# Kernel tuning notes

Measured on AMD Instinct MI355X. Metric: run time of the kernel, lower is better.

## Reference

```python
import jax, jax.numpy as jnp
import numpy as np

ALPHA = 1.0
BETA = 0.25
NUM_EMBEDS = 8192
EMBED_DIM = 512
B, T = 32, 256


def setup_inputs() -> dict:
    key = jax.random.key(0)
    k1, k2 = jax.random.split(key)
    z_e = jax.random.normal(k1, (B, EMBED_DIM, T), dtype=jnp.float32)
    codebook = jax.random.normal(k2, (NUM_EMBEDS, EMBED_DIM), dtype=jnp.float32)
    return {"z_e": z_e, "codebook": codebook}


def reference(z_e, codebook):
    # z_e: (b, d, t) -> (b, t, d)
    z = jnp.transpose(z_e, (0, 2, 1))
    b, t, d = z.shape
    flat = z.reshape(-1, d)  # (N, d), N = b*t

    # squared euclidean distances to every codebook vector: (N, K)
    dists = (
        jnp.sum(flat * flat, axis=1, keepdims=True)
        + jnp.sum(codebook * codebook, axis=1)
        - 2.0 * flat @ codebook.T
    )
    idx = jnp.argmin(dists, axis=1)  # (N,)

    # codebook lookup (equivalent to one-hot @ codebook)
    z_q = codebook[idx].reshape(b, t, d)

    # commitment loss (codebook is EMA-updated, so only e_latent term)
    e_latent_loss = jnp.mean((jax.lax.stop_gradient(z_q) - z) ** 2)
    vq_loss = ALPHA * BETA * e_latent_loss

    # straight-through estimator
    z_q_st = z + jax.lax.stop_gradient(z_q - z)
    z_q_out = jnp.transpose(z_q_st, (0, 2, 1))  # back to (b, d, t)

    # perplexity from mean one-hot assignment probabilities
    counts = jnp.zeros((codebook.shape[0],), dtype=jnp.float32).at[idx].add(1.0)
    avg_probs = counts / flat.shape[0]
    perplexity = jnp.exp(-jnp.sum(avg_probs * jnp.log(avg_probs + 1e-10)))

    return z_q_out, vq_loss, perplexity
```

## Files before the change

kernel.cpp:

```cpp
#include <hip/hip_runtime.h>
#include <stdint.h>

typedef _Float16 half8 __attribute__((ext_vector_type(8)));
typedef float floatx16 __attribute__((ext_vector_type(16)));
typedef unsigned long long u64;

#define ALPHA_ 1.0f
#define BETA_ 0.25f
#define NUM_EMBEDS 8192
#define EMBED_DIM 512
#define B_ 32
#define T_ 256
#define N_TOK 8192
#define THR_GAP 2e-3f


typedef __attribute__((address_space(1))) const void ga_void;
typedef __attribute__((address_space(3))) void ls_void;
__device__ __forceinline__ void gl_lds16(const void* g, void* l) {
    __builtin_amdgcn_global_load_lds((ga_void*)g, (ls_void*)l, 16, 0, 0);
}

__device__ __forceinline__ uint32_t mono(float s) {
    uint32_t u = __float_as_uint(s);
    return (u & 0x80000000u) ? ~u : (u | 0x80000000u);
}
__device__ __forceinline__ float unmono(uint32_t v) {
    return __uint_as_float((v & 0x80000000u) ? (v ^ 0x80000000u) : ~v);
}

__global__ void pack_cb_kernel(const float* __restrict__ cb, _Float16* __restrict__ ci,
                               float* __restrict__ cnorm) {
    int row = blockIdx.x * 4 + (threadIdx.x >> 6);
    int lane = threadIdx.x & 63;
    const float* src = cb + (size_t)row * EMBED_DIM + lane * 8;
    float4 v0 = *(const float4*)src;
    float4 v1 = *(const float4*)(src + 4);
    float x[8] = {v0.x, v0.y, v0.z, v0.w, v1.x, v1.y, v1.z, v1.w};
    half8 hh, mm;
    float s = 0.f;
#pragma unroll
    for (int j = 0; j < 8; ++j) {
        s += x[j] * x[j];
        _Float16 hv = (_Float16)x[j];
        hh[j] = hv;
        mm[j] = (_Float16)((x[j] - (float)hv) * 2048.0f);
    }
    _Float16* dst = ci + (size_t)row * 1024 + lane * 16;
    *(half8*)dst = hh;
    *(half8*)(dst + 8) = mm;
#pragma unroll
    for (int d = 32; d; d >>= 1) s += __shfl_xor(s, d, 64);
    if (lane == 0) cnorm[row] = s;
}

__global__ void pack_z_kernel(const float* __restrict__ z, _Float16* __restrict__ zi) {
    int tid = threadIdx.x;
    int lane = tid & 63, ds = tid >> 6;
    int b = blockIdx.x >> 2;
    int t = ((blockIdx.x & 3) << 6) + lane;
    size_t n = (size_t)b * T_ + t;
    for (int g = 0; g < 16; ++g) {
        int d0 = g * 32 + ds * 8;
        const float* src = z + ((size_t)b * EMBED_DIM + d0) * T_ + t;
        half8 hh, mm;
#pragma unroll
        for (int j = 0; j < 8; ++j) {
            float x = -2.0f * src[(size_t)j * T_];
            _Float16 hv = (_Float16)x;
            hh[j] = hv;
            mm[j] = (_Float16)((x - (float)hv) * 2048.0f);
        }
        _Float16* dst = zi + n * 1024 + (size_t)(g * 4 + ds) * 16;
        *(half8*)dst = hh;
        *(half8*)(dst + 8) = mm;
    }
}

#define MFMA16(a, b, c) __builtin_amdgcn_mfma_f32_32x32x16_f16(a, b, c, 0, 0, 0)

__global__ __launch_bounds__(256, 2) void argmin_kernel(
    const _Float16* __restrict__ cb_i, const _Float16* __restrict__ zt_i,
    const float* __restrict__ cnorm, u64* __restrict__ slot_m1,
    _Float16* __restrict__ slot_d) {
    __shared__ _Float16 As[2][8192];
    __shared__ _Float16 Bs[2][8192];
    __shared__ u64 sK[128];
    __shared__ float sV1[128], sV2[128];
    const int tid = threadIdx.x;
    const int l = tid & 63;
    const int wv = tid >> 6;
    const int l31 = l & 31;
    const int hf = l >> 5;
    const int wp = wv >> 1, wq = wv & 1;
    const int n0 = blockIdx.x * 128;
    const int c0 = blockIdx.y * 128;

    const bool isA = wv < 2;
    const _Float16* gsrc = isA ? cb_i : zt_i;
    const int rbase = (isA ? c0 : n0) + ((wv & 1) << 6);
    const int srow = l >> 3;
    const int sseg = (l & 7) ^ srow;
    const size_t lanefix = (size_t)(rbase + srow) * 1024 + sseg * 8;

    floatx16 acc1[2][2], acc2[2][2];
#pragma unroll
    for (int a = 0; a < 2; ++a)
#pragma unroll
        for (int b = 0; b < 2; ++b)
#pragma unroll
            for (int r = 0; r < 16; ++r) { acc1[a][b][r] = 0.f; acc2[a][b][r] = 0.f; }

    auto stage = [&](int p, int s) {
        const _Float16* gs = gsrc + lanefix + (size_t)s * 64;
        _Float16* lb = (isA ? As[p] : Bs[p]) + ((wv & 1) << 12);
#pragma unroll
        for (int j = 0; j < 8; ++j)
            gl_lds16(gs + (size_t)j * 8192, lb + j * 512);
    };

    stage(0, 0);
    __syncthreads();
    for (int s = 0; s < 16; ++s) {
        const int p = s & 1;
        if (s < 15) stage(p ^ 1, s + 1);
        const _Float16* Ab = As[p] + (wp * 64 + l31) * 64;
        const _Float16* Bb = Bs[p] + (wq * 64 + l31) * 64;
        const int rs = l31 & 7;
#pragma unroll
        for (int kk = 0; kk < 2; ++kk) {
            const int j = kk * 2 + hf;
            const int ph = ((2 * j) ^ rs) * 8;
            const int pm = ((2 * j + 1) ^ rs) * 8;
            half8 Ah0 = *(const half8*)(Ab + ph), Am0 = *(const half8*)(Ab + pm);
            half8 Ah1 = *(const half8*)(Ab + 2048 + ph), Am1 = *(const half8*)(Ab + 2048 + pm);
            half8 Bh0 = *(const half8*)(Bb + ph), Bm0 = *(const half8*)(Bb + pm);
            half8 Bh1 = *(const half8*)(Bb + 2048 + ph), Bm1 = *(const half8*)(Bb + 2048 + pm);
            acc1[0][0] = MFMA16(Ah0, Bh0, acc1[0][0]);
            acc2[0][0] = MFMA16(Ah0, Bm0, acc2[0][0]);
            acc2[0][0] = MFMA16(Am0, Bh0, acc2[0][0]);
            acc1[0][1] = MFMA16(Ah0, Bh1, acc1[0][1]);
            acc2[0][1] = MFMA16(Ah0, Bm1, acc2[0][1]);
            acc2[0][1] = MFMA16(Am0, Bh1, acc2[0][1]);
            acc1[1][0] = MFMA16(Ah1, Bh0, acc1[1][0]);
            acc2[1][0] = MFMA16(Ah1, Bm0, acc2[1][0]);
            acc2[1][0] = MFMA16(Am1, Bh0, acc2[1][0]);
            acc1[1][1] = MFMA16(Ah1, Bh1, acc1[1][1]);
            acc2[1][1] = MFMA16(Ah1, Bm1, acc2[1][1]);
            acc2[1][1] = MFMA16(Am1, Bh1, acc2[1][1]);
        }
        __syncthreads();
    }

    u64 km[2]; float kv1[2], kv2[2];
#pragma unroll
    for (int qi = 0; qi < 2; ++qi) {
        u64 m1k = ~0ULL;
        float m1v = 3.4e38f, m2 = 3.4e38f;
#pragma unroll
        for (int ti = 0; ti < 2; ++ti)
#pragma unroll
            for (int g = 0; g < 4; ++g) {
                const int cb4 = c0 + wp * 64 + ti * 32 + g * 8 + hf * 4;
                float4 cn = *(const float4*)(cnorm + cb4);
                const floatx16& A1 = acc1[ti][qi];
                const floatx16& A2 = acc2[ti][qi];
                float sv[4] = {cn.x + A1[g * 4 + 0] + A2[g * 4 + 0] * (1.0f / 2048.0f),
                               cn.y + A1[g * 4 + 1] + A2[g * 4 + 1] * (1.0f / 2048.0f),
                               cn.z + A1[g * 4 + 2] + A2[g * 4 + 2] * (1.0f / 2048.0f),
                               cn.w + A1[g * 4 + 3] + A2[g * 4 + 3] * (1.0f / 2048.0f)};
#pragma unroll
                for (int q = 0; q < 4; ++q) {
                    u64 key = ((u64)mono(sv[q]) << 32) | (uint32_t)(cb4 + q);
                    if (key < m1k) { m2 = m1v; m1v = sv[q]; m1k = key; }
                    else m2 = fminf(m2, sv[q]);
                }
            }
        u64 ok = __shfl_xor(m1k, 32, 64);
        float ov = __shfl_xor(m1v, 32, 64);
        float om2 = __shfl_xor(m2, 32, 64);
        if (ok < m1k) { m2 = fminf(fminf(m2, om2), m1v); m1v = ov; m1k = ok; }
        else m2 = fminf(fminf(m2, om2), ov);
        km[qi] = m1k; kv1[qi] = m1v; kv2[qi] = m2;
    }
    if (wp == 1 && hf == 0) {
#pragma unroll
        for (int qi = 0; qi < 2; ++qi) {
            int idx = wq * 64 + qi * 32 + l31;
            sK[idx] = km[qi]; sV1[idx] = kv1[qi]; sV2[idx] = kv2[qi];
        }
    }
    __syncthreads();
    if (wp == 0 && hf == 0) {
#pragma unroll
        for (int qi = 0; qi < 2; ++qi) {
            int idx = wq * 64 + qi * 32 + l31;
            u64 m1k = km[qi]; float m1v = kv1[qi], m2 = kv2[qi];
            u64 ok = sK[idx]; float ov = sV1[idx], om2 = sV2[idx];
            if (ok < m1k) { m2 = fminf(fminf(m2, om2), m1v); m1v = ov; m1k = ok; }
            else m2 = fminf(fminf(m2, om2), ov);
            int tok = n0 + idx;
            slot_m1[((size_t)blockIdx.y << 13) + tok] = m1k;
            slot_d[((size_t)blockIdx.y << 13) + tok] = (_Float16)(m2 - m1v);
        }
    }
}

__global__ void combine_kernel(const u64* __restrict__ slot_m1, const _Float16* __restrict__ slot_d,
                               u64* __restrict__ wexact, int* __restrict__ worklist,
                               int* __restrict__ nflag) {
    int tok = blockIdx.x * 256 + threadIdx.x;
    u64 g1 = ~0ULL;
    float g1v = 3.4e38f, g2 = 3.4e38f;
    for (int c = 0; c < 64; ++c) {
        u64 k = slot_m1[((size_t)c << 13) + tok];
        float kv = unmono((uint32_t)(k >> 32));
        float v2 = kv + (float)slot_d[((size_t)c << 13) + tok];
        if (k < g1) { g2 = fminf(g2, g1v); g1 = k; g1v = kv; }
        else g2 = fminf(g2, kv);
        g2 = fminf(g2, v2);
    }
    if (g2 - g1v > THR_GAP) wexact[tok] = g1;
    else { int i = atomicAdd(nflag, 1); if (i < 8192) worklist[i] = tok; }
}

__global__ void fallback_kernel(const float* __restrict__ z, const float* __restrict__ cb,
                                const float* __restrict__ cnorm,
                                const int* __restrict__ worklist, const int* __restrict__ nflag,
                                u64* __restrict__ wexact) {
    int n = *nflag;
    if (n > 8192) n = 8192;
    const int l = threadIdx.x & 63, wv = threadIdx.x >> 6;
    const int cbase = blockIdx.x * 128;
    for (int fi = blockIdx.y; fi < n; fi += gridDim.y) {
        int tok = worklist[fi];
        int b = tok >> 8, t = tok & 255;
        const float* zp = z + ((size_t)b * EMBED_DIM) * T_ + t;
        float zr[8];
#pragma unroll
        for (int j = 0; j < 8; ++j) zr[j] = zp[(size_t)(l * 8 + j) * T_];
        u64 m1 = ~0ULL;
        for (int j = 0; j < 32; ++j) {
            int c = cbase + wv + j * 4;
            const float* cp = cb + (size_t)c * EMBED_DIM + l * 8;
            float4 a = *(const float4*)cp, bb = *(const float4*)(cp + 4);
            float dot = zr[0] * a.x + zr[1] * a.y + zr[2] * a.z + zr[3] * a.w +
                        zr[4] * bb.x + zr[5] * bb.y + zr[6] * bb.z + zr[7] * bb.w;
#pragma unroll
            for (int m = 32; m; m >>= 1) dot += __shfl_xor(dot, m, 64);
            if (l == 0) {
                float s = cnorm[c] - 2.0f * dot;
                u64 key = ((u64)mono(s) << 32) | (uint32_t)c;
                if (key < m1) m1 = key;
            }
        }
        if (l == 0) atomicMin(&wexact[tok], m1);
    }
}

__global__ void gather_kernel(const float* __restrict__ z, const float* __restrict__ cb,
                              const u64* __restrict__ wexact,
                              float* __restrict__ out, int* __restrict__ counts,
                              float* __restrict__ sse_acc) {
    __shared__ unsigned int sIdx[64];
    __shared__ float red[4];
    const int tid = threadIdx.x;
    const int n0 = blockIdx.x * 64;
    const int b = n0 >> 8;
    const int t0 = n0 & 255;
    if (tid < 64) {
        unsigned int idx = (unsigned int)(wexact[n0 + tid] & 0xffffffffULL);
        sIdx[tid] = idx;
        atomicAdd(&counts[idx], 1);
    }
    __syncthreads();
    const int w = tid >> 6;
    const int lane = tid & 63;
    const float* crow = cb + (size_t)sIdx[lane] * EMBED_DIM;
    const size_t base = ((size_t)b * EMBED_DIM) * T_ + (size_t)(t0 + lane);
    float sse = 0.f;
    for (int d = w; d < EMBED_DIM; d += 4) {
        float v = crow[d];
        size_t o = base + (size_t)d * T_;
        float diff = v - z[o];
        out[o] = v;
        sse += diff * diff;
    }
    for (int m = 32; m; m >>= 1) sse += __shfl_xor(sse, m, 64);
    if (lane == 0) red[w] = sse;
    __syncthreads();
    if (tid == 0) atomicAdd(sse_acc, red[0] + red[1] + red[2] + red[3]);
}

__global__ void finalize_kernel(const int* __restrict__ counts,
                                const float* __restrict__ sse_acc,
                                float* __restrict__ out) {
    __shared__ float red[4];
    const int tid = threadIdx.x;
    float e = 0.f;
    for (int k = tid; k < NUM_EMBEDS; k += 256) {
        float p = (float)counts[k] * (1.0f / (float)N_TOK);
        e += p * logf(p + 1e-10f);
    }
    for (int m = 32; m; m >>= 1) e += __shfl_xor(e, m, 64);
    if ((tid & 63) == 0) red[tid >> 6] = e;
    __syncthreads();
    if (tid == 0) {
        float ent = red[0] + red[1] + red[2] + red[3];
        size_t off = (size_t)B_ * EMBED_DIM * T_;
        out[off + 0] = (ALPHA_ * BETA_) * sse_acc[0] / (float)((size_t)N_TOK * EMBED_DIM);
        out[off + 1] = expf(-ent);
    }
}

extern "C" void kernel_launch(void* const* d_in, const int* in_sizes, int n_in,
                              void* d_out, int out_size, void* d_ws, size_t ws_size,
                              hipStream_t stream) {
    const float* z = (const float*)d_in[0];
    const float* cb = (const float*)d_in[1];
    float* out = (float*)d_out;
    char* ws = (char*)d_ws;
    u64* wexact = (u64*)ws;
    float* cnorm = (float*)(ws + 65536);
    int* counts = (int*)(ws + 98304);
    float* sse = (float*)(ws + 131072);
    int* nflag = (int*)(ws + 131076);
    int* worklist = (int*)(ws + 131080);
    u64* slot_m1 = (u64*)(ws + (1ull << 20));
    _Float16* slot_d = (_Float16*)(ws + (5ull << 20));
    _Float16* cb_i = (_Float16*)(ws + (6ull << 20));
    _Float16* zt_i = (_Float16*)(ws + (22ull << 20));

    hipMemsetAsync(wexact, 0xFF, NUM_EMBEDS * sizeof(u64), stream);
    hipMemsetAsync(counts, 0, NUM_EMBEDS * sizeof(int) + 8, stream);

    pack_cb_kernel<<<NUM_EMBEDS / 4, 256, 0, stream>>>(cb, cb_i, cnorm);
    pack_z_kernel<<<N_TOK / 64, 256, 0, stream>>>(z, zt_i);
    argmin_kernel<<<dim3(N_TOK / 128, NUM_EMBEDS / 128), 256, 0, stream>>>(cb_i, zt_i, cnorm, slot_m1, slot_d);
    combine_kernel<<<N_TOK / 256, 256, 0, stream>>>(slot_m1, slot_d, wexact, worklist, nflag);
    fallback_kernel<<<dim3(64, 16), 256, 0, stream>>>(z, cb, cnorm, worklist, nflag, wexact);
    gather_kernel<<<N_TOK / 64, 256, 0, stream>>>(z, cb, wexact, out, counts, sse);
    finalize_kernel<<<1, 256, 0, stream>>>(counts, sse, out);
}
```

Measured before the change: 363.5 us.

## Enlarge argmin tile to 256x128 with 8 waves and ping-pong MFMA scheduling

The argmin GEMM block tile grows from 128x128 to 256 codebook rows by 128 tokens, using 512 threads (8 waves) and a single fused 96KB double-buffered LDS region loaded by all waves. The k-loop is split into two half-steps, with explicit s_barrier, waitcnt and setprio so waves alternate between LDS reads and MFMA bursts while the global-to-LDS prefetch is in flight. The cross-wave reduction now merges four wave rows, and combine_kernel reads 32 partial slots instead of 64. This aims for more operand reuse per loaded byte and better overlap of loads with matrix math, at the cost of heavier LDS use, lower occupancy and fragile hand-placed barriers.

```diff
diff --git a/kernel.cpp b/kernel.cpp
--- a/kernel.cpp
+++ b/kernel.cpp
@@ -79,29 +79,35 @@
 
 #define MFMA16(a, b, c) __builtin_amdgcn_mfma_f32_32x32x16_f16(a, b, c, 0, 0, 0)
 
-__global__ __launch_bounds__(256, 2) void argmin_kernel(
+__global__ __launch_bounds__(512, 2) void argmin_kernel(
     const _Float16* __restrict__ cb_i, const _Float16* __restrict__ zt_i,
     const float* __restrict__ cnorm, u64* __restrict__ slot_m1,
     _Float16* __restrict__ slot_d) {
-    __shared__ _Float16 As[2][8192];
-    __shared__ _Float16 Bs[2][8192];
-    __shared__ u64 sK[128];
-    __shared__ float sV1[128], sV2[128];
+    __shared__ alignas(16) _Float16 Sm[2][24576];
+    __shared__ u64 sK[3][128];
+    __shared__ float sV1[3][128], sV2[3][128];
+
     const int tid = threadIdx.x;
     const int l = tid & 63;
     const int wv = tid >> 6;
     const int l31 = l & 31;
     const int hf = l >> 5;
-    const int wp = wv >> 1, wq = wv & 1;
+    const int wm = wv >> 1;
+    const int wn = wv & 1;
     const int n0 = blockIdx.x * 128;
-    const int c0 = blockIdx.y * 128;
-
-    const bool isA = wv < 2;
-    const _Float16* gsrc = isA ? cb_i : zt_i;
-    const int rbase = (isA ? c0 : n0) + ((wv & 1) << 6);
+    const int c0 = blockIdx.y * 256;
+
     const int srow = l >> 3;
     const int sseg = (l & 7) ^ srow;
-    const size_t lanefix = (size_t)(rbase + srow) * 1024 + sseg * 8;
+    const _Float16* gsrc[6];
+#pragma unroll
+    for (int j = 0; j < 6; ++j) {
+        int c = wv * 6 + j;
+        gsrc[j] = (c < 32)
+                      ? cb_i + (size_t)(c0 + c * 8 + srow) * 1024 + sseg * 8
+                      : zt_i + (size_t)(n0 + (c - 32) * 8 + srow) * 1024 + sseg * 8;
+    }
+    const int sloff = wv * 3072;
 
     floatx16 acc1[2][2], acc2[2][2];
 #pragma unroll
@@ -111,31 +117,42 @@
 #pragma unroll
             for (int r = 0; r < 16; ++r) { acc1[a][b][r] = 0.f; acc2[a][b][r] = 0.f; }
 
-    auto stage = [&](int p, int s) {
-        const _Float16* gs = gsrc + lanefix + (size_t)s * 64;
-        _Float16* lb = (isA ? As[p] : Bs[p]) + ((wv & 1) << 12);
-#pragma unroll
-        for (int j = 0; j < 8; ++j)
-            gl_lds16(gs + (size_t)j * 8192, lb + j * 512);
-    };
-
-    stage(0, 0);
-    __syncthreads();
-    for (int s = 0; s < 16; ++s) {
-        const int p = s & 1;
-        if (s < 15) stage(p ^ 1, s + 1);
-        const _Float16* Ab = As[p] + (wp * 64 + l31) * 64;
-        const _Float16* Bb = Bs[p] + (wq * 64 + l31) * 64;
-        const int rs = l31 & 7;
-#pragma unroll
-        for (int kk = 0; kk < 2; ++kk) {
-            const int j = kk * 2 + hf;
-            const int ph = ((2 * j) ^ rs) * 8;
-            const int pm = ((2 * j + 1) ^ rs) * 8;
-            half8 Ah0 = *(const half8*)(Ab + ph), Am0 = *(const half8*)(Ab + pm);
-            half8 Ah1 = *(const half8*)(Ab + 2048 + ph), Am1 = *(const half8*)(Ab + 2048 + pm);
-            half8 Bh0 = *(const half8*)(Bb + ph), Bm0 = *(const half8*)(Bb + pm);
-            half8 Bh1 = *(const half8*)(Bb + 2048 + ph), Bm1 = *(const half8*)(Bb + 2048 + pm);
+    const int rs = l31 & 7;
+    const int goh0 = ((2 * hf) ^ rs) * 8;
+    const int gom0 = ((2 * hf + 1) ^ rs) * 8;
+    const int goh1 = ((4 + 2 * hf) ^ rs) * 8;
+    const int gom1 = ((4 + 2 * hf + 1) ^ rs) * 8;
+    const int aoff = (wm * 64 + l31) * 64;
+    const int boff = 16384 + (wn * 64 + l31) * 64;
+
+#pragma unroll
+    for (int j = 0; j < 6; ++j) gl_lds16(gsrc[j], &Sm[0][sloff + j * 512]);
+    asm volatile("s_waitcnt vmcnt(0)" ::: "memory");
+    __builtin_amdgcn_s_barrier();
+
+    for (int t = 0; t < 16; ++t) {
+        const int p = t & 1;
+        const _Float16* Ap = &Sm[0][0] + p * 24576 + aoff;
+        const _Float16* Bp = &Sm[0][0] + p * 24576 + boff;
+        _Float16* snx = &Sm[0][0] + (p ^ 1) * 24576 + sloff;
+        {
+            half8 Ah0 = *(const half8*)(Ap + goh0);
+            half8 Am0 = *(const half8*)(Ap + gom0);
+            half8 Ah1 = *(const half8*)(Ap + 2048 + goh0);
+            half8 Am1 = *(const half8*)(Ap + 2048 + gom0);
+            half8 Bh0 = *(const half8*)(Bp + goh0);
+            half8 Bm0 = *(const half8*)(Bp + gom0);
+            half8 Bh1 = *(const half8*)(Bp + 2048 + goh0);
+            half8 Bm1 = *(const half8*)(Bp + 2048 + gom0);
+            if (t < 15) {
+#pragma unroll
+                for (int j = 0; j < 6; ++j)
+                    gl_lds16(gsrc[j] + (size_t)(t + 1) * 64, snx + j * 512);
+            }
+            __builtin_amdgcn_s_barrier();
+            asm volatile("s_waitcnt lgkmcnt(0)" ::: "memory");
+            __builtin_amdgcn_sched_barrier(0);
+            __builtin_amdgcn_s_setprio(1);
             acc1[0][0] = MFMA16(Ah0, Bh0, acc1[0][0]);
             acc2[0][0] = MFMA16(Ah0, Bm0, acc2[0][0]);
             acc2[0][0] = MFMA16(Am0, Bh0, acc2[0][0]);
@@ -148,8 +165,38 @@
             acc1[1][1] = MFMA16(Ah1, Bh1, acc1[1][1]);
             acc2[1][1] = MFMA16(Ah1, Bm1, acc2[1][1]);
             acc2[1][1] = MFMA16(Am1, Bh1, acc2[1][1]);
-        }
-        __syncthreads();
+            __builtin_amdgcn_s_setprio(0);
+            __builtin_amdgcn_s_barrier();
+        }
+        {
+            half8 Ah0 = *(const half8*)(Ap + goh1);
+            half8 Am0 = *(const half8*)(Ap + gom1);
+            half8 Ah1 = *(const half8*)(Ap + 2048 + goh1);
+            half8 Am1 = *(const half8*)(Ap + 2048 + gom1);
+            half8 Bh0 = *(const half8*)(Bp + goh1);
+            half8 Bm0 = *(const half8*)(Bp + gom1);
+            half8 Bh1 = *(const half8*)(Bp + 2048 + goh1);
+            half8 Bm1 = *(const half8*)(Bp + 2048 + gom1);
+            __builtin_amdgcn_s_barrier();
+            asm volatile("s_waitcnt lgkmcnt(0)" ::: "memory");
+            __builtin_amdgcn_sched_barrier(0);
+            __builtin_amdgcn_s_setprio(1);
+            acc1[0][0] = MFMA16(Ah0, Bh0, acc1[0][0]);
+            acc2[0][0] = MFMA16(Ah0, Bm0, acc2[0][0]);
+            acc2[0][0] = MFMA16(Am0, Bh0, acc2[0][0]);
+            acc1[0][1] = MFMA16(Ah0, Bh1, acc1[0][1]);
+            acc2[0][1] = MFMA16(Ah0, Bm1, acc2[0][1]);
+            acc2[0][1] = MFMA16(Am0, Bh1, acc2[0][1]);
+            acc1[1][0] = MFMA16(Ah1, Bh0, acc1[1][0]);
+            acc2[1][0] = MFMA16(Ah1, Bm0, acc2[1][0]);
+            acc2[1][0] = MFMA16(Am1, Bh0, acc2[1][0]);
+            acc1[1][1] = MFMA16(Ah1, Bh1, acc1[1][1]);
+            acc2[1][1] = MFMA16(Ah1, Bm1, acc2[1][1]);
+            acc2[1][1] = MFMA16(Am1, Bh1, acc2[1][1]);
+            __builtin_amdgcn_s_setprio(0);
+            asm volatile("s_waitcnt vmcnt(0)" ::: "memory");
+            __builtin_amdgcn_s_barrier();
+        }
     }
 
     u64 km[2]; float kv1[2], kv2[2];
@@ -161,7 +208,7 @@
         for (int ti = 0; ti < 2; ++ti)
 #pragma unroll
             for (int g = 0; g < 4; ++g) {
-                const int cb4 = c0 + wp * 64 + ti * 32 + g * 8 + hf * 4;
+                const int cb4 = c0 + wm * 64 + ti * 32 + g * 8 + hf * 4;
                 float4 cn = *(const float4*)(cnorm + cb4);
                 const floatx16& A1 = acc1[ti][qi];
                 const floatx16& A2 = acc2[ti][qi];
@@ -183,22 +230,25 @@
         else m2 = fminf(fminf(m2, om2), ov);
         km[qi] = m1k; kv1[qi] = m1v; kv2[qi] = m2;
     }
-    if (wp == 1 && hf == 0) {
+    if (wm != 0 && hf == 0) {
 #pragma unroll
         for (int qi = 0; qi < 2; ++qi) {
-            int idx = wq * 64 + qi * 32 + l31;
-            sK[idx] = km[qi]; sV1[idx] = kv1[qi]; sV2[idx] = kv2[qi];
+            int idx = wn * 64 + qi * 32 + l31;
+            sK[wm - 1][idx] = km[qi]; sV1[wm - 1][idx] = kv1[qi]; sV2[wm - 1][idx] = kv2[qi];
         }
     }
     __syncthreads();
-    if (wp == 0 && hf == 0) {
+    if (wm == 0 && hf == 0) {
 #pragma unroll
         for (int qi = 0; qi < 2; ++qi) {
-            int idx = wq * 64 + qi * 32 + l31;
+            int idx = wn * 64 + qi * 32 + l31;
             u64 m1k = km[qi]; float m1v = kv1[qi], m2 = kv2[qi];
-            u64 ok = sK[idx]; float ov = sV1[idx], om2 = sV2[idx];
-            if (ok < m1k) { m2 = fminf(fminf(m2, om2), m1v); m1v = ov; m1k = ok; }
-            else m2 = fminf(fminf(m2, om2), ov);
+#pragma unroll
+            for (int j = 0; j < 3; ++j) {
+                u64 ok = sK[j][idx]; float ov = sV1[j][idx], om2 = sV2[j][idx];
+                if (ok < m1k) { m2 = fminf(fminf(m2, om2), m1v); m1v = ov; m1k = ok; }
+                else m2 = fminf(fminf(m2, om2), ov);
+            }
             int tok = n0 + idx;
             slot_m1[((size_t)blockIdx.y << 13) + tok] = m1k;
             slot_d[((size_t)blockIdx.y << 13) + tok] = (_Float16)(m2 - m1v);
@@ -212,7 +262,7 @@
     int tok = blockIdx.x * 256 + threadIdx.x;
     u64 g1 = ~0ULL;
     float g1v = 3.4e38f, g2 = 3.4e38f;
-    for (int c = 0; c < 64; ++c) {
+    for (int c = 0; c < 32; ++c) {
         u64 k = slot_m1[((size_t)c << 13) + tok];
         float kv = unmono((uint32_t)(k >> 32));
         float v2 = kv + (float)slot_d[((size_t)c << 13) + tok];
@@ -336,7 +386,7 @@
 
     pack_cb_kernel<<<NUM_EMBEDS / 4, 256, 0, stream>>>(cb, cb_i, cnorm);
     pack_z_kernel<<<N_TOK / 64, 256, 0, stream>>>(z, zt_i);
-    argmin_kernel<<<dim3(N_TOK / 128, NUM_EMBEDS / 128), 256, 0, stream>>>(cb_i, zt_i, cnorm, slot_m1, slot_d);
+    argmin_kernel<<<dim3(N_TOK / 128, NUM_EMBEDS / 256), 512, 0, stream>>>(cb_i, zt_i, cnorm, slot_m1, slot_d);
     combine_kernel<<<N_TOK / 256, 256, 0, stream>>>(slot_m1, slot_d, wexact, worklist, nflag);
     fallback_kernel<<<dim3(64, 16), 256, 0, stream>>>(z, cb, cnorm, worklist, nflag, wexact);
     gather_kernel<<<N_TOK / 64, 256, 0, stream>>>(z, cb, wexact, out, counts, sse);
```

Result: slower. 376.5 us (+3.6%).

## Load MFMA fragments directly from pre-swizzled global layout instead of LDS staging

Applied to the files above, without the earlier changes.

Packing kernels now write codebook and token data in an MFMA-fragment-ordered layout, so each lane reads its half8 operands directly from global memory with contiguous per-lane addresses. The argmin kernel drops LDS double buffering and its barriers, and uses 512-thread blocks where each of 8 waves owns 32 codebook rows against 128 tokens, with register double-buffered loads. Per-block codebook coverage doubles to 256, which halves the number of partial slots the combine kernel reduces. This trades LDS traffic and syncs for repeated global/L2 reads of the token tile across waves and exposed global latency.

```diff
diff --git a/kernel.cpp b/kernel.cpp
--- a/kernel.cpp
+++ b/kernel.cpp
@@ -15,12 +15,6 @@
 #define THR_GAP 2e-3f
 
 
-typedef __attribute__((address_space(1))) const void ga_void;
-typedef __attribute__((address_space(3))) void ls_void;
-__device__ __forceinline__ void gl_lds16(const void* g, void* l) {
-    __builtin_amdgcn_global_load_lds((ga_void*)g, (ls_void*)l, 16, 0, 0);
-}
-
 __device__ __forceinline__ uint32_t mono(float s) {
     uint32_t u = __float_as_uint(s);
     return (u & 0x80000000u) ? ~u : (u | 0x80000000u);
@@ -29,11 +23,11 @@
     return __uint_as_float((v & 0x80000000u) ? (v ^ 0x80000000u) : ~v);
 }
 
-__global__ void pack_cb_kernel(const float* __restrict__ cb, _Float16* __restrict__ ci,
+__global__ void pack_cb_kernel(const float* __restrict__ cb, _Float16* __restrict__ cf,
                                float* __restrict__ cnorm) {
     int row = blockIdx.x * 4 + (threadIdx.x >> 6);
-    int lane = threadIdx.x & 63;
-    const float* src = cb + (size_t)row * EMBED_DIM + lane * 8;
+    int l = threadIdx.x & 63;
+    const float* src = cb + (size_t)row * EMBED_DIM + l * 8;
     float4 v0 = *(const float4*)src;
     float4 v1 = *(const float4*)(src + 4);
     float x[8] = {v0.x, v0.y, v0.z, v0.w, v1.x, v1.y, v1.z, v1.w};
@@ -46,20 +40,26 @@
         hh[j] = hv;
         mm[j] = (_Float16)((x[j] - (float)hv) * 2048.0f);
     }
-    _Float16* dst = ci + (size_t)row * 1024 + lane * 16;
-    *(half8*)dst = hh;
-    *(half8*)(dst + 8) = mm;
+    int s_ = l >> 2, kk = (l >> 1) & 1, hfb = l & 1;
+    int slot0 = s_ * 4 + kk * 2;
+    size_t base = (size_t)(row >> 5) * 32768 + (size_t)slot0 * 512 +
+                  (size_t)((row & 31) + hfb * 32) * 8;
+    *(half8*)(cf + base) = hh;
+    *(half8*)(cf + base + 512) = mm;
 #pragma unroll
     for (int d = 32; d; d >>= 1) s += __shfl_xor(s, d, 64);
-    if (lane == 0) cnorm[row] = s;
-}
-
-__global__ void pack_z_kernel(const float* __restrict__ z, _Float16* __restrict__ zi) {
+    if (l == 0) cnorm[row] = s;
+}
+
+__global__ void pack_z_kernel(const float* __restrict__ z, _Float16* __restrict__ zf) {
     int tid = threadIdx.x;
-    int lane = tid & 63, ds = tid >> 6;
-    int b = blockIdx.x >> 2;
-    int t = ((blockIdx.x & 3) << 6) + lane;
-    size_t n = (size_t)b * T_ + t;
+    int l = tid & 63, ds = tid >> 6;
+    int n = blockIdx.x * 64 + l;
+    int b = n >> 8, t = n & 255;
+    int kk = ds >> 1, hfb = ds & 1;
+    int tb = n >> 7, q = (n >> 5) & 3;
+    size_t lanebase = (size_t)tb * 131072 + (size_t)q * 512 +
+                      (size_t)((n & 31) + hfb * 32) * 8;
     for (int g = 0; g < 16; ++g) {
         int d0 = g * 32 + ds * 8;
         const float* src = z + ((size_t)b * EMBED_DIM + d0) * T_ + t;
@@ -71,138 +71,119 @@
             hh[j] = hv;
             mm[j] = (_Float16)((x - (float)hv) * 2048.0f);
         }
-        _Float16* dst = zi + n * 1024 + (size_t)(g * 4 + ds) * 16;
+        int slot0 = g * 4 + kk * 2;
+        _Float16* dst = zf + lanebase + (size_t)slot0 * 2048;
         *(half8*)dst = hh;
-        *(half8*)(dst + 8) = mm;
+        *(half8*)(dst + 2048) = mm;
     }
 }
 
 #define MFMA16(a, b, c) __builtin_amdgcn_mfma_f32_32x32x16_f16(a, b, c, 0, 0, 0)
 
-__global__ __launch_bounds__(256, 2) void argmin_kernel(
-    const _Float16* __restrict__ cb_i, const _Float16* __restrict__ zt_i,
+#define LOADSET(X, hs)                                                              \
+    X##Ah = *(const half8*)(Ab + ((hs)*2 + 0) * 512 + lane8);                       \
+    X##Am = *(const half8*)(Ab + ((hs)*2 + 1) * 512 + lane8);                       \
+    _Pragma("unroll") for (int q_ = 0; q_ < 4; ++q_) {                              \
+        X##Bh[q_] = *(const half8*)(Bb + (((hs)*2 + 0) * 4 + q_) * 512 + lane8);    \
+        X##Bm[q_] = *(const half8*)(Bb + (((hs)*2 + 1) * 4 + q_) * 512 + lane8);    \
+    }
+
+#define MFMASET(X)                                                                  \
+    _Pragma("unroll") for (int q_ = 0; q_ < 4; ++q_)                                \
+        acc1[q_] = MFMA16(X##Ah, X##Bh[q_], acc1[q_]);                              \
+    _Pragma("unroll") for (int q_ = 0; q_ < 4; ++q_)                                \
+        acc2[q_] = MFMA16(X##Ah, X##Bm[q_], acc2[q_]);                              \
+    _Pragma("unroll") for (int q_ = 0; q_ < 4; ++q_)                                \
+        acc2[q_] = MFMA16(X##Am, X##Bh[q_], acc2[q_]);
+
+__global__ __launch_bounds__(512, 2) void argmin_kernel(
+    const _Float16* __restrict__ cb_f, const _Float16* __restrict__ zt_f,
     const float* __restrict__ cnorm, u64* __restrict__ slot_m1,
     _Float16* __restrict__ slot_d) {
-    __shared__ _Float16 As[2][8192];
-    __shared__ _Float16 Bs[2][8192];
-    __shared__ u64 sK[128];
-    __shared__ float sV1[128], sV2[128];
+    __shared__ u64 sK[8][128];
+    __shared__ float sV1[8][128], sV2[8][128];
+
     const int tid = threadIdx.x;
     const int l = tid & 63;
     const int wv = tid >> 6;
     const int l31 = l & 31;
     const int hf = l >> 5;
-    const int wp = wv >> 1, wq = wv & 1;
-    const int n0 = blockIdx.x * 128;
-    const int c0 = blockIdx.y * 128;
-
-    const bool isA = wv < 2;
-    const _Float16* gsrc = isA ? cb_i : zt_i;
-    const int rbase = (isA ? c0 : n0) + ((wv & 1) << 6);
-    const int srow = l >> 3;
-    const int sseg = (l & 7) ^ srow;
-    const size_t lanefix = (size_t)(rbase + srow) * 1024 + sseg * 8;
-
-    floatx16 acc1[2][2], acc2[2][2];
-#pragma unroll
-    for (int a = 0; a < 2; ++a)
-#pragma unroll
-        for (int b = 0; b < 2; ++b)
-#pragma unroll
-            for (int r = 0; r < 16; ++r) { acc1[a][b][r] = 0.f; acc2[a][b][r] = 0.f; }
-
-    auto stage = [&](int p, int s) {
-        const _Float16* gs = gsrc + lanefix + (size_t)s * 64;
-        _Float16* lb = (isA ? As[p] : Bs[p]) + ((wv & 1) << 12);
-#pragma unroll
-        for (int j = 0; j < 8; ++j)
-            gl_lds16(gs + (size_t)j * 8192, lb + j * 512);
-    };
-
-    stage(0, 0);
-    __syncthreads();
-    for (int s = 0; s < 16; ++s) {
-        const int p = s & 1;
-        if (s < 15) stage(p ^ 1, s + 1);
-        const _Float16* Ab = As[p] + (wp * 64 + l31) * 64;
-        const _Float16* Bb = Bs[p] + (wq * 64 + l31) * 64;
-        const int rs = l31 & 7;
-#pragma unroll
-        for (int kk = 0; kk < 2; ++kk) {
-            const int j = kk * 2 + hf;
-            const int ph = ((2 * j) ^ rs) * 8;
-            const int pm = ((2 * j + 1) ^ rs) * 8;
-            half8 Ah0 = *(const half8*)(Ab + ph), Am0 = *(const half8*)(Ab + pm);
-            half8 Ah1 = *(const half8*)(Ab + 2048 + ph), Am1 = *(const half8*)(Ab + 2048 + pm);
-            half8 Bh0 = *(const half8*)(Bb + ph), Bm0 = *(const half8*)(Bb + pm);
-            half8 Bh1 = *(const half8*)(Bb + 2048 + ph), Bm1 = *(const half8*)(Bb + 2048 + pm);
-            acc1[0][0] = MFMA16(Ah0, Bh0, acc1[0][0]);
-            acc2[0][0] = MFMA16(Ah0, Bm0, acc2[0][0]);
-            acc2[0][0] = MFMA16(Am0, Bh0, acc2[0][0]);
-            acc1[0][1] = MFMA16(Ah0, Bh1, acc1[0][1]);
-            acc2[0][1] = MFMA16(Ah0, Bm1, acc2[0][1]);
-            acc2[0][1] = MFMA16(Am0, Bh1, acc2[0][1]);
-            acc1[1][0] = MFMA16(Ah1, Bh0, acc1[1][0]);
-            acc2[1][0] = MFMA16(Ah1, Bm0, acc2[1][0]);
-            acc2[1][0] = MFMA16(Am1, Bh0, acc2[1][0]);
-            acc1[1][1] = MFMA16(Ah1, Bh1, acc1[1][1]);
-            acc2[1][1] = MFMA16(Ah1, Bm1, acc2[1][1]);
-            acc2[1][1] = MFMA16(Am1, Bh1, acc2[1][1]);
-        }
-        __syncthreads();
-    }
-
-    u64 km[2]; float kv1[2], kv2[2];
-#pragma unroll
-    for (int qi = 0; qi < 2; ++qi) {
+    const int tb = blockIdx.x;
+    const int c0 = blockIdx.y * 256;
+    const int cb32 = blockIdx.y * 8 + wv;
+
+    const _Float16* Ab = cb_f + (size_t)cb32 * 32768;
+    const _Float16* Bb = zt_f + (size_t)tb * 131072;
+    const int lane8 = l * 8;
+
+    floatx16 acc1[4], acc2[4];
+#pragma unroll
+    for (int q = 0; q < 4; ++q)
+#pragma unroll
+        for (int r = 0; r < 16; ++r) { acc1[q][r] = 0.f; acc2[q][r] = 0.f; }
+
+    half8 cAh, cAm, cBh[4], cBm[4];
+    half8 nAh, nAm, nBh[4], nBm[4];
+
+    LOADSET(c, 0);
+    for (int hs = 0; hs < 30; hs += 2) {
+        LOADSET(n, hs + 1);
+        MFMASET(c);
+        LOADSET(c, hs + 2);
+        MFMASET(n);
+    }
+    LOADSET(n, 31);
+    MFMASET(c);
+    MFMASET(n);
+
+    const int cb0 = c0 + wv * 32;
+    u64 km[4]; float kv1[4], kv2[4];
+#pragma unroll
+    for (int q = 0; q < 4; ++q) {
         u64 m1k = ~0ULL;
         float m1v = 3.4e38f, m2 = 3.4e38f;
 #pragma unroll
-        for (int ti = 0; ti < 2; ++ti)
-#pragma unroll
-            for (int g = 0; g < 4; ++g) {
-                const int cb4 = c0 + wp * 64 + ti * 32 + g * 8 + hf * 4;
-                float4 cn = *(const float4*)(cnorm + cb4);
-                const floatx16& A1 = acc1[ti][qi];
-                const floatx16& A2 = acc2[ti][qi];
-                float sv[4] = {cn.x + A1[g * 4 + 0] + A2[g * 4 + 0] * (1.0f / 2048.0f),
-                               cn.y + A1[g * 4 + 1] + A2[g * 4 + 1] * (1.0f / 2048.0f),
-                               cn.z + A1[g * 4 + 2] + A2[g * 4 + 2] * (1.0f / 2048.0f),
-                               cn.w + A1[g * 4 + 3] + A2[g * 4 + 3] * (1.0f / 2048.0f)};
-#pragma unroll
-                for (int q = 0; q < 4; ++q) {
-                    u64 key = ((u64)mono(sv[q]) << 32) | (uint32_t)(cb4 + q);
-                    if (key < m1k) { m2 = m1v; m1v = sv[q]; m1k = key; }
-                    else m2 = fminf(m2, sv[q]);
-                }
+        for (int g = 0; g < 4; ++g) {
+            const int cb4 = cb0 + g * 8 + hf * 4;
+            float4 cn = *(const float4*)(cnorm + cb4);
+            float sv[4] = {cn.x + acc1[q][g * 4 + 0] + acc2[q][g * 4 + 0] * (1.0f / 2048.0f),
+                           cn.y + acc1[q][g * 4 + 1] + acc2[q][g * 4 + 1] * (1.0f / 2048.0f),
+                           cn.z + acc1[q][g * 4 + 2] + acc2[q][g * 4 + 2] * (1.0f / 2048.0f),
+                           cn.w + acc1[q][g * 4 + 3] + acc2[q][g * 4 + 3] * (1.0f / 2048.0f)};
+#pragma unroll
+            for (int r = 0; r < 4; ++r) {
+                u64 key = ((u64)mono(sv[r]) << 32) | (uint32_t)(cb4 + r);
+                if (key < m1k) { m2 = m1v; m1v = sv[r]; m1k = key; }
+                else m2 = fminf(m2, sv[r]);
             }
+        }
         u64 ok = __shfl_xor(m1k, 32, 64);
         float ov = __shfl_xor(m1v, 32, 64);
         float om2 = __shfl_xor(m2, 32, 64);
         if (ok < m1k) { m2 = fminf(fminf(m2, om2), m1v); m1v = ov; m1k = ok; }
         else m2 = fminf(fminf(m2, om2), ov);
-        km[qi] = m1k; kv1[qi] = m1v; kv2[qi] = m2;
-    }
-    if (wp == 1 && hf == 0) {
-#pragma unroll
-        for (int qi = 0; qi < 2; ++qi) {
-            int idx = wq * 64 + qi * 32 + l31;
-            sK[idx] = km[qi]; sV1[idx] = kv1[qi]; sV2[idx] = kv2[qi];
+        km[q] = m1k; kv1[q] = m1v; kv2[q] = m2;
+    }
+    if (hf == 0) {
+#pragma unroll
+        for (int q = 0; q < 4; ++q) {
+            int idx = q * 32 + l31;
+            sK[wv][idx] = km[q]; sV1[wv][idx] = kv1[q]; sV2[wv][idx] = kv2[q];
         }
     }
     __syncthreads();
-    if (wp == 0 && hf == 0) {
-#pragma unroll
-        for (int qi = 0; qi < 2; ++qi) {
-            int idx = wq * 64 + qi * 32 + l31;
-            u64 m1k = km[qi]; float m1v = kv1[qi], m2 = kv2[qi];
-            u64 ok = sK[idx]; float ov = sV1[idx], om2 = sV2[idx];
+    if (tid < 128) {
+        u64 m1k = ~0ULL;
+        float m1v = 3.4e38f, m2 = 3.4e38f;
+#pragma unroll
+        for (int w = 0; w < 8; ++w) {
+            u64 ok = sK[w][tid]; float ov = sV1[w][tid], om2 = sV2[w][tid];
             if (ok < m1k) { m2 = fminf(fminf(m2, om2), m1v); m1v = ov; m1k = ok; }
             else m2 = fminf(fminf(m2, om2), ov);
-            int tok = n0 + idx;
-            slot_m1[((size_t)blockIdx.y << 13) + tok] = m1k;
-            slot_d[((size_t)blockIdx.y << 13) + tok] = (_Float16)(m2 - m1v);
-        }
+        }
+        int tok = tb * 128 + tid;
+        slot_m1[((size_t)blockIdx.y << 13) + tok] = m1k;
+        slot_d[((size_t)blockIdx.y << 13) + tok] = (_Float16)(m2 - m1v);
     }
 }
 
@@ -212,7 +193,7 @@
     int tok = blockIdx.x * 256 + threadIdx.x;
     u64 g1 = ~0ULL;
     float g1v = 3.4e38f, g2 = 3.4e38f;
-    for (int c = 0; c < 64; ++c) {
+    for (int c = 0; c < 32; ++c) {
         u64 k = slot_m1[((size_t)c << 13) + tok];
         float kv = unmono((uint32_t)(k >> 32));
         float v2 = kv + (float)slot_d[((size_t)c << 13) + tok];
@@ -328,15 +309,15 @@
     int* worklist = (int*)(ws + 131080);
     u64* slot_m1 = (u64*)(ws + (1ull << 20));
     _Float16* slot_d = (_Float16*)(ws + (5ull << 20));
-    _Float16* cb_i = (_Float16*)(ws + (6ull << 20));
-    _Float16* zt_i = (_Float16*)(ws + (22ull << 20));
+    _Float16* cb_f = (_Float16*)(ws + (6ull << 20));
+    _Float16* zt_f = (_Float16*)(ws + (22ull << 20));
 
     hipMemsetAsync(wexact, 0xFF, NUM_EMBEDS * sizeof(u64), stream);
     hipMemsetAsync(counts, 0, NUM_EMBEDS * sizeof(int) + 8, stream);
 
-    pack_cb_kernel<<<NUM_EMBEDS / 4, 256, 0, stream>>>(cb, cb_i, cnorm);
-    pack_z_kernel<<<N_TOK / 64, 256, 0, stream>>>(z, zt_i);
-    argmin_kernel<<<dim3(N_TOK / 128, NUM_EMBEDS / 128), 256, 0, stream>>>(cb_i, zt_i, cnorm, slot_m1, slot_d);
+    pack_cb_kernel<<<NUM_EMBEDS / 4, 256, 0, stream>>>(cb, cb_f, cnorm);
+    pack_z_kernel<<<N_TOK / 64, 256, 0, stream>>>(z, zt_f);
+    argmin_kernel<<<dim3(N_TOK / 128, NUM_EMBEDS / 256), 512, 0, stream>>>(cb_f, zt_f, cnorm, slot_m1, slot_d);
     combine_kernel<<<N_TOK / 256, 256, 0, stream>>>(slot_m1, slot_d, wexact, worklist, nflag);
     fallback_kernel<<<dim3(64, 16), 256, 0, stream>>>(z, cb, cnorm, worklist, nflag, wexact);
     gather_kernel<<<N_TOK / 64, 256, 0, stream>>>(z, cb, wexact, out, counts, sse);
```

Measured after the change: 373.2 us. 2.7% more time.
